# Optimization experiments

Measured on AMD Instinct MI355X. Metric: run time of the kernel, lower is better.

Reference implementation:

```python
import jax, jax.numpy as jnp
import numpy as np

B, LC, LQ, D = 64, 512, 64, 256

def setup_inputs() -> dict:
    key = jax.random.key(0)
    k1, k2, k3, k4 = jax.random.split(key, 4)
    contex = jax.random.normal(k1, (B, LC, D), dtype=jnp.float32)
    question = jax.random.normal(k2, (B, LQ, D), dtype=jnp.float32)
    W_weight = jax.random.normal(k3, (1, 3 * D), dtype=jnp.float32) * (1.0 / np.sqrt(3 * D))
    W_bias = jax.random.normal(k4, (1,), dtype=jnp.float32) * 0.01
    return {"contex": contex, "question": question, "W_weight": W_weight, "W_bias": W_bias}

def reference(contex, question, W_weight, W_bias):
    d = contex.shape[-1]
    w = W_weight[0]  # [3D]; cat order in original is [q, c, q*c]
    wq, wc, wi = w[:d], w[d:2 * d], w[2 * d:]
    # S[b,i,j] = c_i.wc + q_j.wq + (c_i*q_j).wi + bias  (trilinear decomposition)
    s_c = contex @ wc                                   # [B, Lc]
    s_q = question @ wq                                 # [B, Lq]
    s_i = jnp.einsum('bid,bjd->bij', contex * wi, question)  # [B, Lc, Lq]
    S = s_i + s_c[:, :, None] + s_q[:, None, :] + W_bias[0]
    S1 = jax.nn.softmax(S, axis=2)                      # over question
    S2 = jax.nn.softmax(S, axis=1)                      # over context
    A = jnp.einsum('bij,bjd->bid', S1, question)        # [B, Lc, D]
    S3 = jnp.einsum('bij,bkj->bik', S1, S2)             # [B, Lc, Lc]
    Bm = jnp.einsum('bik,bkd->bid', S3, contex)         # [B, Lc, D]
    out = jnp.concatenate([contex, A, contex * A, contex * Bm], axis=2)  # [B, Lc, 4D]
    return out  # dropout is identity at inference
```

## Files before the change

### kernel.cpp

```cpp
#include <hip/hip_runtime.h>

#define BB 64
#define LCC 512
#define LQQ 64
#define DDD 256

typedef short bf16x8 __attribute__((ext_vector_type(8)));
typedef float f32x4 __attribute__((ext_vector_type(4)));

__device__ __forceinline__ unsigned short f2bf(float f) {
  union { float f; unsigned u; } v; v.f = f;
  unsigned u = v.u;
  return (unsigned short)((u + 0x7fffu + ((u >> 16) & 1u)) >> 16);
}
__device__ __forceinline__ float bf2f(unsigned u16) {
  union { unsigned u; float f; } v; v.u = u16 << 16;
  return v.f;
}

__global__ __launch_bounds__(256) void k1_scores(
    const float* __restrict__ cx, const float* __restrict__ qu,
    const float* __restrict__ W, const float* __restrict__ Wb,
    unsigned short* __restrict__ E, unsigned short* __restrict__ Et,
    float* __restrict__ rinv)
{
  __shared__ float w_lds[768];
  __shared__ unsigned short As[128 * 72];
  __shared__ unsigned short Bs[64 * 72];
  __shared__ float E_lds[128 * 65];
  __shared__ float sc_lds[128];
  __shared__ float sq_lds[64];
  float* red = E_lds;

  const int tid = threadIdx.x;
  const int b  = blockIdx.x >> 2;
  const int i0 = (blockIdx.x & 3) * 128;
  const int w = tid >> 6, lane = tid & 63, quad = lane >> 4, ln = lane & 15;

  for (int idx = tid; idx < 768; idx += 256) w_lds[idx] = W[idx];
  __syncthreads();

  {
    const int i = tid >> 1, h = tid & 1;
    const float4* src = (const float4*)(cx + ((size_t)(b * LCC + i0 + i)) * DDD + h * 128);
    const float* wc = w_lds + 256 + h * 128;
    float s = 0.f;
#pragma unroll
    for (int u = 0; u < 32; ++u) {
      float4 v = src[u];
      s += v.x * wc[u*4+0] + v.y * wc[u*4+1] + v.z * wc[u*4+2] + v.w * wc[u*4+3];
    }
    red[tid] = s;
  }
  __syncthreads();
  if (tid < 128) sc_lds[tid] = red[2*tid] + red[2*tid+1];
  __syncthreads();
  if (tid < 128) {
    const int j = tid >> 1, h = tid & 1;
    const float4* src = (const float4*)(qu + ((size_t)(b * LQQ + j)) * DDD + h * 128);
    const float* wq = w_lds + h * 128;
    float s = 0.f;
#pragma unroll
    for (int u = 0; u < 32; ++u) {
      float4 v = src[u];
      s += v.x * wq[u*4+0] + v.y * wq[u*4+1] + v.z * wq[u*4+2] + v.w * wq[u*4+3];
    }
    red[tid] = s;
  }
  __syncthreads();
  if (tid < 64) sq_lds[tid] = red[2*tid] + red[2*tid+1];

  f32x4 acc[2][4];
#pragma unroll
  for (int a = 0; a < 2; ++a)
#pragma unroll
    for (int c = 0; c < 4; ++c) acc[a][c] = (f32x4){0.f, 0.f, 0.f, 0.f};

  for (int kk = 0; kk < 4; ++kk) {
    __syncthreads();
    {
      const int i = tid >> 1, h = tid & 1;
      const float4* src = (const float4*)(cx + ((size_t)(b * LCC + i0 + i)) * DDD + kk * 64 + h * 32);
      const float* wi = w_lds + 512 + kk * 64 + h * 32;
      unsigned short* dst = As + i * 72 + h * 32;
#pragma unroll
      for (int u = 0; u < 8; ++u) {
        float4 v = src[u];
        ushort4 o;
        o.x = f2bf(v.x * wi[u*4+0]);
        o.y = f2bf(v.y * wi[u*4+1]);
        o.z = f2bf(v.z * wi[u*4+2]);
        o.w = f2bf(v.w * wi[u*4+3]);
        *(ushort4*)(dst + u * 4) = o;
      }
    }
    {
      const int j = tid >> 2, c = tid & 3;
      const float4* src = (const float4*)(qu + ((size_t)(b * LQQ + j)) * DDD + kk * 64 + c * 16);
      unsigned short* dst = Bs + j * 72 + c * 16;
#pragma unroll
      for (int u = 0; u < 4; ++u) {
        float4 v = src[u];
        ushort4 o = { f2bf(v.x), f2bf(v.y), f2bf(v.z), f2bf(v.w) };
        *(ushort4*)(dst + u * 4) = o;
      }
    }
    __syncthreads();
#pragma unroll
    for (int ks = 0; ks < 2; ++ks) {
      bf16x8 af[2];
#pragma unroll
      for (int tm = 0; tm < 2; ++tm)
        af[tm] = *(const bf16x8*)(As + (w * 32 + tm * 16 + ln) * 72 + ks * 32 + quad * 8);
#pragma unroll
      for (int tn = 0; tn < 4; ++tn) {
        bf16x8 bf = *(const bf16x8*)(Bs + (tn * 16 + ln) * 72 + ks * 32 + quad * 8);
#pragma unroll
        for (int tm = 0; tm < 2; ++tm)
          acc[tm][tn] = __builtin_amdgcn_mfma_f32_16x16x32_bf16(af[tm], bf, acc[tm][tn], 0, 0, 0);
      }
    }
  }

  const float bias = Wb[0];
  __syncthreads();
#pragma unroll
  for (int tm = 0; tm < 2; ++tm)
#pragma unroll
    for (int tn = 0; tn < 4; ++tn)
#pragma unroll
      for (int r = 0; r < 4; ++r) {
        int il = w * 32 + tm * 16 + quad * 4 + r;
        int j  = tn * 16 + ln;
        float e = __expf(acc[tm][tn][r] + sc_lds[il] + sq_lds[j] + bias);
        E_lds[il * 65 + j] = e;
      }
  __syncthreads();
  if (tid < 128) {
    float s = 0.f;
#pragma unroll
    for (int j = 0; j < 64; ++j) s += E_lds[tid * 65 + j];
    rinv[b * LCC + i0 + tid] = 1.0f / s;
  }
  {
    const int i = tid >> 1, h = tid & 1;
    unsigned short* dst = E + ((size_t)(b * LCC + i0 + i)) * 64 + h * 32;
    const float* srcr = E_lds + i * 65 + h * 32;
#pragma unroll
    for (int u = 0; u < 8; ++u) {
      ushort4 o = { f2bf(srcr[u*4+0]), f2bf(srcr[u*4+1]), f2bf(srcr[u*4+2]), f2bf(srcr[u*4+3]) };
      *(ushort4*)(dst + u * 4) = o;
    }
  }
  {
    const int j = tid >> 2, c = tid & 3;
    unsigned short* dst = Et + ((size_t)(b * LQQ + j)) * LCC + i0 + c * 32;
#pragma unroll
    for (int u = 0; u < 8; ++u) {
      ushort4 o;
      o.x = f2bf(E_lds[(c*32 + u*4 + 0) * 65 + j]);
      o.y = f2bf(E_lds[(c*32 + u*4 + 1) * 65 + j]);
      o.z = f2bf(E_lds[(c*32 + u*4 + 2) * 65 + j]);
      o.w = f2bf(E_lds[(c*32 + u*4 + 3) * 65 + j]);
      *(ushort4*)(dst + u * 4) = o;
    }
  }
}

__global__ __launch_bounds__(256) void k2_tmat(
    const float* __restrict__ cx, const float* __restrict__ qu,
    const unsigned short* __restrict__ Et,
    unsigned short* __restrict__ Qt, unsigned short* __restrict__ Tt)
{
  __shared__ unsigned short As2[64 * 72];
  __shared__ unsigned short Bs2[64 * 72];
  __shared__ float Tl[64 * 65];
  __shared__ float cs_lds[64];

  const int tid = threadIdx.x;
  const int b  = blockIdx.x >> 2;
  const int d0 = (blockIdx.x & 3) * 64;
  const int w = tid >> 6, lane = tid & 63, quad = lane >> 4, ln = lane & 15;

  {
    const int j = tid >> 2, c = tid & 3;
    const float4* src = (const float4*)(qu + ((size_t)(b * LQQ + j)) * DDD + d0 + c * 16);
#pragma unroll
    for (int u = 0; u < 4; ++u) {
      float4 v = src[u];
      Tl[j * 65 + c*16 + u*4 + 0] = v.x;
      Tl[j * 65 + c*16 + u*4 + 1] = v.y;
      Tl[j * 65 + c*16 + u*4 + 2] = v.z;
      Tl[j * 65 + c*16 + u*4 + 3] = v.w;
    }
  }
  __syncthreads();
  {
    const int d = tid & 63, cj = tid >> 6;
    unsigned short* dst = Qt + ((size_t)(b * DDD + d0 + d)) * 64 + cj * 16;
#pragma unroll
    for (int u = 0; u < 4; ++u) {
      ushort4 o;
      o.x = f2bf(Tl[(cj*16 + u*4 + 0) * 65 + d]);
      o.y = f2bf(Tl[(cj*16 + u*4 + 1) * 65 + d]);
      o.z = f2bf(Tl[(cj*16 + u*4 + 2) * 65 + d]);
      o.w = f2bf(Tl[(cj*16 + u*4 + 3) * 65 + d]);
      *(ushort4*)(dst + u * 4) = o;
    }
  }

  f32x4 acc[4];
#pragma unroll
  for (int c = 0; c < 4; ++c) acc[c] = (f32x4){0.f, 0.f, 0.f, 0.f};
  float csp = 0.f;

  const int sj = tid >> 2, sc = tid & 3;
  const int si = tid & 63, sc2 = tid >> 6;

  for (int kk = 0; kk < 8; ++kk) {
    __syncthreads();
    {
      const uint4* src = (const uint4*)(Et + ((size_t)(b * LQQ + sj)) * LCC + kk * 64 + sc * 16);
#pragma unroll
      for (int u = 0; u < 2; ++u) {
        uint4 raw = src[u];
        *(uint4*)(As2 + sj * 72 + sc * 16 + u * 8) = raw;
        csp += bf2f(raw.x & 0xffffu) + bf2f(raw.x >> 16)
             + bf2f(raw.y & 0xffffu) + bf2f(raw.y >> 16)
             + bf2f(raw.z & 0xffffu) + bf2f(raw.z >> 16)
             + bf2f(raw.w & 0xffffu) + bf2f(raw.w >> 16);
      }
    }
    {
      const float4* src = (const float4*)(cx + ((size_t)(b * LCC + kk * 64 + si)) * DDD + d0 + sc2 * 16);
#pragma unroll
      for (int u = 0; u < 4; ++u) {
        float4 v = src[u];
        Bs2[(sc2*16 + u*4 + 0) * 72 + si] = f2bf(v.x);
        Bs2[(sc2*16 + u*4 + 1) * 72 + si] = f2bf(v.y);
        Bs2[(sc2*16 + u*4 + 2) * 72 + si] = f2bf(v.z);
        Bs2[(sc2*16 + u*4 + 3) * 72 + si] = f2bf(v.w);
      }
    }
    __syncthreads();
#pragma unroll
    for (int ks = 0; ks < 2; ++ks) {
      bf16x8 af = *(const bf16x8*)(As2 + (w * 16 + ln) * 72 + ks * 32 + quad * 8);
#pragma unroll
      for (int tn = 0; tn < 4; ++tn) {
        bf16x8 bf = *(const bf16x8*)(Bs2 + (tn * 16 + ln) * 72 + ks * 32 + quad * 8);
        acc[tn] = __builtin_amdgcn_mfma_f32_16x16x32_bf16(af, bf, acc[tn], 0, 0, 0);
      }
    }
  }

  __syncthreads();
  Tl[tid] = csp;
  __syncthreads();
  if (tid < 64) {
    float s = Tl[4*tid] + Tl[4*tid+1] + Tl[4*tid+2] + Tl[4*tid+3];
    cs_lds[tid] = 1.0f / s;
  }
  __syncthreads();
#pragma unroll
  for (int tn = 0; tn < 4; ++tn)
#pragma unroll
    for (int r = 0; r < 4; ++r) {
      int jl = w * 16 + quad * 4 + r;
      Tl[jl * 65 + tn * 16 + ln] = acc[tn][r] * cs_lds[jl];
    }
  __syncthreads();
  {
    const int d = tid & 63, cj = tid >> 6;
    unsigned short* dst = Tt + ((size_t)(b * DDD + d0 + d)) * 64 + cj * 16;
#pragma unroll
    for (int u = 0; u < 4; ++u) {
      ushort4 o;
      o.x = f2bf(Tl[(cj*16 + u*4 + 0) * 65 + d]);
      o.y = f2bf(Tl[(cj*16 + u*4 + 1) * 65 + d]);
      o.z = f2bf(Tl[(cj*16 + u*4 + 2) * 65 + d]);
      o.w = f2bf(Tl[(cj*16 + u*4 + 3) * 65 + d]);
      *(ushort4*)(dst + u * 4) = o;
    }
  }
}

__global__ __launch_bounds__(256) void k3_out(
    const float* __restrict__ cx,
    const unsigned short* __restrict__ E,
    const unsigned short* __restrict__ Qt,
    const unsigned short* __restrict__ Tt,
    const float* __restrict__ rinv,
    float* __restrict__ out)
{
  __shared__ unsigned short As3[64 * 72];
  __shared__ unsigned short Bs3[256 * 72];
  __shared__ float ri_lds[64];

  const int tid = threadIdx.x;
  const int bid = blockIdx.x;
  const int b    = bid >> 4;
  const int it   = (bid >> 1) & 7;
  const int half = bid & 1;
  const int i0 = it * 64;
  const int w = tid >> 6, lane = tid & 63, quad = lane >> 4, ln = lane & 15;

  {
    const int i = tid >> 2, c = tid & 3;
    const uint4* src = (const uint4*)(E + ((size_t)(b * LCC + i0 + i)) * 64 + c * 16);
#pragma unroll
    for (int u = 0; u < 2; ++u)
      *(uint4*)(As3 + i * 72 + c * 16 + u * 8) = src[u];
  }
  {
    const unsigned short* Bsrc = half ? Tt : Qt;
    const int nb = tid & 63, c2 = tid >> 6;
#pragma unroll
    for (int rr = 0; rr < 4; ++rr) {
      int n = rr * 64 + nb;
      const uint4* src = (const uint4*)(Bsrc + ((size_t)(b * DDD + n)) * 64 + c2 * 16);
#pragma unroll
      for (int u = 0; u < 2; ++u)
        *(uint4*)(Bs3 + n * 72 + c2 * 16 + u * 8) = src[u];
    }
  }
  if (tid < 64) ri_lds[tid] = rinv[b * LCC + i0 + tid];
  __syncthreads();

  f32x4 acc[4][4];
#pragma unroll
  for (int a = 0; a < 4; ++a)
#pragma unroll
    for (int c = 0; c < 4; ++c) acc[a][c] = (f32x4){0.f, 0.f, 0.f, 0.f};

#pragma unroll
  for (int ks = 0; ks < 2; ++ks) {
    bf16x8 af[4], bf[4];
#pragma unroll
    for (int tm = 0; tm < 4; ++tm)
      af[tm] = *(const bf16x8*)(As3 + (tm * 16 + ln) * 72 + ks * 32 + quad * 8);
#pragma unroll
    for (int tn = 0; tn < 4; ++tn)
      bf[tn] = *(const bf16x8*)(Bs3 + (w * 64 + tn * 16 + ln) * 72 + ks * 32 + quad * 8);
#pragma unroll
    for (int tm = 0; tm < 4; ++tm)
#pragma unroll
      for (int tn = 0; tn < 4; ++tn)
        acc[tm][tn] = __builtin_amdgcn_mfma_f32_16x16x32_bf16(af[tm], bf[tn], acc[tm][tn], 0, 0, 0);
  }

  const float* cxb = cx + (size_t)b * LCC * DDD;
  float* ob = out + (size_t)b * LCC * 1024;
#pragma unroll
  for (int tm = 0; tm < 4; ++tm)
#pragma unroll
    for (int tn = 0; tn < 4; ++tn)
#pragma unroll
      for (int r = 0; r < 4; ++r) {
        int il = tm * 16 + quad * 4 + r;
        int i = i0 + il;
        int n = w * 64 + tn * 16 + ln;
        float v = acc[tm][tn][r] * ri_lds[il];
        float c = cxb[(size_t)i * DDD + n];
        if (half == 0) {
          ob[(size_t)i * 1024 + 256 + n] = v;
          ob[(size_t)i * 1024 + 512 + n] = c * v;
        } else {
          ob[(size_t)i * 1024 + n]       = c;
          ob[(size_t)i * 1024 + 768 + n] = c * v;
        }
      }
}

extern "C" void kernel_launch(void* const* d_in, const int* in_sizes, int n_in,
                              void* d_out, int out_size, void* d_ws, size_t ws_size,
                              hipStream_t stream) {
  const float* cx = (const float*)d_in[0];
  const float* qu = (const float*)d_in[1];
  const float* W  = (const float*)d_in[2];
  const float* Wb = (const float*)d_in[3];
  float* out = (float*)d_out;

  char* wsb = (char*)d_ws;
  unsigned short* E   = (unsigned short*)(wsb);
  unsigned short* Et  = (unsigned short*)(wsb + (4ull << 20));
  unsigned short* Qt  = (unsigned short*)(wsb + (8ull << 20));
  unsigned short* Tt  = (unsigned short*)(wsb + (10ull << 20));
  float*          ri  = (float*)(wsb + (12ull << 20));

  k1_scores<<<dim3(256), dim3(256), 0, stream>>>(cx, qu, W, Wb, E, Et, ri);
  k2_tmat  <<<dim3(256), dim3(256), 0, stream>>>(cx, qu, Et, Qt, Tt);
  k3_out   <<<dim3(1024), dim3(256), 0, stream>>>(cx, E, Qt, Tt, ri, out);
}
```

Before: 208.6 us.

## Fuse score projections into GEMM staging and vectorize output stores via LDS

In the scores kernel, the c·wc and q·wq row projections are now accumulated while the context and question tiles are staged for the MFMA. This drops the separate pre-pass that read each row a second time, and the row-sum reduction now uses all 256 threads. In the output kernel, accumulator fragments are transposed through LDS (reusing the B-operand buffer) so each thread writes contiguous float4 rows for the output and reads context as float4. The cost is extra LDS traffic and barriers per 16-row chunk.

New measurement: 199.6 us. 1.04x faster.

```diff
diff --git a/kernel.cpp b/kernel.cpp
--- a/kernel.cpp
+++ b/kernel.cpp
@@ -30,7 +30,6 @@
   __shared__ float E_lds[128 * 65];
   __shared__ float sc_lds[128];
   __shared__ float sq_lds[64];
-  float* red = E_lds;
 
   const int tid = threadIdx.x;
   const int b  = blockIdx.x >> 2;
@@ -38,37 +37,6 @@
   const int w = tid >> 6, lane = tid & 63, quad = lane >> 4, ln = lane & 15;
 
   for (int idx = tid; idx < 768; idx += 256) w_lds[idx] = W[idx];
-  __syncthreads();
-
-  {
-    const int i = tid >> 1, h = tid & 1;
-    const float4* src = (const float4*)(cx + ((size_t)(b * LCC + i0 + i)) * DDD + h * 128);
-    const float* wc = w_lds + 256 + h * 128;
-    float s = 0.f;
-#pragma unroll
-    for (int u = 0; u < 32; ++u) {
-      float4 v = src[u];
-      s += v.x * wc[u*4+0] + v.y * wc[u*4+1] + v.z * wc[u*4+2] + v.w * wc[u*4+3];
-    }
-    red[tid] = s;
-  }
-  __syncthreads();
-  if (tid < 128) sc_lds[tid] = red[2*tid] + red[2*tid+1];
-  __syncthreads();
-  if (tid < 128) {
-    const int j = tid >> 1, h = tid & 1;
-    const float4* src = (const float4*)(qu + ((size_t)(b * LQQ + j)) * DDD + h * 128);
-    const float* wq = w_lds + h * 128;
-    float s = 0.f;
-#pragma unroll
-    for (int u = 0; u < 32; ++u) {
-      float4 v = src[u];
-      s += v.x * wq[u*4+0] + v.y * wq[u*4+1] + v.z * wq[u*4+2] + v.w * wq[u*4+3];
-    }
-    red[tid] = s;
-  }
-  __syncthreads();
-  if (tid < 64) sq_lds[tid] = red[2*tid] + red[2*tid+1];
 
   f32x4 acc[2][4];
 #pragma unroll
@@ -76,16 +44,22 @@
 #pragma unroll
     for (int c = 0; c < 4; ++c) acc[a][c] = (f32x4){0.f, 0.f, 0.f, 0.f};
 
+  float scp = 0.f;
+  float sqp = 0.f;
+  const int ai = tid >> 1, ah = tid & 1;
+  const int bj = tid >> 2, bc = tid & 3;
+
   for (int kk = 0; kk < 4; ++kk) {
     __syncthreads();
     {
-      const int i = tid >> 1, h = tid & 1;
-      const float4* src = (const float4*)(cx + ((size_t)(b * LCC + i0 + i)) * DDD + kk * 64 + h * 32);
-      const float* wi = w_lds + 512 + kk * 64 + h * 32;
-      unsigned short* dst = As + i * 72 + h * 32;
+      const float4* src = (const float4*)(cx + ((size_t)(b * LCC + i0 + ai)) * DDD + kk * 64 + ah * 32);
+      const float* wi = w_lds + 512 + kk * 64 + ah * 32;
+      const float* wc = w_lds + 256 + kk * 64 + ah * 32;
+      unsigned short* dst = As + ai * 72 + ah * 32;
 #pragma unroll
       for (int u = 0; u < 8; ++u) {
         float4 v = src[u];
+        scp += v.x * wc[u*4+0] + v.y * wc[u*4+1] + v.z * wc[u*4+2] + v.w * wc[u*4+3];
         ushort4 o;
         o.x = f2bf(v.x * wi[u*4+0]);
         o.y = f2bf(v.y * wi[u*4+1]);
@@ -95,12 +69,13 @@
       }
     }
     {
-      const int j = tid >> 2, c = tid & 3;
-      const float4* src = (const float4*)(qu + ((size_t)(b * LQQ + j)) * DDD + kk * 64 + c * 16);
-      unsigned short* dst = Bs + j * 72 + c * 16;
+      const float4* src = (const float4*)(qu + ((size_t)(b * LQQ + bj)) * DDD + kk * 64 + bc * 16);
+      const float* wq = w_lds + kk * 64 + bc * 16;
+      unsigned short* dst = Bs + bj * 72 + bc * 16;
 #pragma unroll
       for (int u = 0; u < 4; ++u) {
         float4 v = src[u];
+        sqp += v.x * wq[u*4+0] + v.y * wq[u*4+1] + v.z * wq[u*4+2] + v.w * wq[u*4+3];
         ushort4 o = { f2bf(v.x), f2bf(v.y), f2bf(v.z), f2bf(v.w) };
         *(ushort4*)(dst + u * 4) = o;
       }
@@ -122,8 +97,17 @@
     }
   }
 
+  __syncthreads();
+  w_lds[tid] = scp;
+  w_lds[256 + tid] = sqp;
+  __syncthreads();
+  if (tid < 128) sc_lds[tid] = w_lds[2*tid] + w_lds[2*tid+1];
+  if (tid < 64)
+    sq_lds[tid] = w_lds[256 + 4*tid] + w_lds[256 + 4*tid+1]
+                + w_lds[256 + 4*tid+2] + w_lds[256 + 4*tid+3];
   const float bias = Wb[0];
   __syncthreads();
+
 #pragma unroll
   for (int tm = 0; tm < 2; ++tm)
 #pragma unroll
@@ -136,16 +120,18 @@
         E_lds[il * 65 + j] = e;
       }
   __syncthreads();
-  if (tid < 128) {
+  {
     float s = 0.f;
 #pragma unroll
-    for (int j = 0; j < 64; ++j) s += E_lds[tid * 65 + j];
-    rinv[b * LCC + i0 + tid] = 1.0f / s;
-  }
-  {
-    const int i = tid >> 1, h = tid & 1;
-    unsigned short* dst = E + ((size_t)(b * LCC + i0 + i)) * 64 + h * 32;
-    const float* srcr = E_lds + i * 65 + h * 32;
+    for (int j = 0; j < 32; ++j) s += E_lds[ai * 65 + ah * 32 + j];
+    w_lds[tid] = s;
+  }
+  __syncthreads();
+  if (tid < 128) rinv[b * LCC + i0 + tid] = 1.0f / (w_lds[2*tid] + w_lds[2*tid+1]);
+
+  {
+    unsigned short* dst = E + ((size_t)(b * LCC + i0 + ai)) * 64 + ah * 32;
+    const float* srcr = E_lds + ai * 65 + ah * 32;
 #pragma unroll
     for (int u = 0; u < 8; ++u) {
       ushort4 o = { f2bf(srcr[u*4+0]), f2bf(srcr[u*4+1]), f2bf(srcr[u*4+2]), f2bf(srcr[u*4+3]) };
@@ -153,15 +139,14 @@
     }
   }
   {
-    const int j = tid >> 2, c = tid & 3;
-    unsigned short* dst = Et + ((size_t)(b * LQQ + j)) * LCC + i0 + c * 32;
+    unsigned short* dst = Et + ((size_t)(b * LQQ + bj)) * LCC + i0 + bc * 32;
 #pragma unroll
     for (int u = 0; u < 8; ++u) {
       ushort4 o;
-      o.x = f2bf(E_lds[(c*32 + u*4 + 0) * 65 + j]);
-      o.y = f2bf(E_lds[(c*32 + u*4 + 1) * 65 + j]);
-      o.z = f2bf(E_lds[(c*32 + u*4 + 2) * 65 + j]);
-      o.w = f2bf(E_lds[(c*32 + u*4 + 3) * 65 + j]);
+      o.x = f2bf(E_lds[(bc*32 + u*4 + 0) * 65 + bj]);
+      o.y = f2bf(E_lds[(bc*32 + u*4 + 1) * 65 + bj]);
+      o.z = f2bf(E_lds[(bc*32 + u*4 + 2) * 65 + bj]);
+      o.w = f2bf(E_lds[(bc*32 + u*4 + 3) * 65 + bj]);
       *(ushort4*)(dst + u * 4) = o;
     }
   }
@@ -294,8 +279,10 @@
     float* __restrict__ out)
 {
   __shared__ unsigned short As3[64 * 72];
-  __shared__ unsigned short Bs3[256 * 72];
+  __shared__ char BsTr[256 * 72 * 2];
   __shared__ float ri_lds[64];
+  unsigned short* Bs3 = (unsigned short*)BsTr;
+  float* Tr = (float*)BsTr;
 
   const int tid = threadIdx.x;
   const int bid = blockIdx.x;
@@ -351,25 +338,36 @@
 
   const float* cxb = cx + (size_t)b * LCC * DDD;
   float* ob = out + (size_t)b * LCC * 1024;
-#pragma unroll
-  for (int tm = 0; tm < 4; ++tm)
+  const int row = tid >> 4;
+  const int fq  = tid & 15;
+
+#pragma unroll
+  for (int tm = 0; tm < 4; ++tm) {
+    __syncthreads();
 #pragma unroll
     for (int tn = 0; tn < 4; ++tn)
 #pragma unroll
       for (int r = 0; r < 4; ++r) {
-        int il = tm * 16 + quad * 4 + r;
-        int i = i0 + il;
-        int n = w * 64 + tn * 16 + ln;
-        float v = acc[tm][tn][r] * ri_lds[il];
-        float c = cxb[(size_t)i * DDD + n];
-        if (half == 0) {
-          ob[(size_t)i * 1024 + 256 + n] = v;
-          ob[(size_t)i * 1024 + 512 + n] = c * v;
-        } else {
-          ob[(size_t)i * 1024 + n]       = c;
-          ob[(size_t)i * 1024 + 768 + n] = c * v;
-        }
-      }
+        int rloc = quad * 4 + r;
+        Tr[rloc * 260 + w * 64 + tn * 16 + ln] = acc[tm][tn][r] * ri_lds[tm * 16 + rloc];
+      }
+    __syncthreads();
+    const int i = i0 + tm * 16 + row;
+#pragma unroll
+    for (int u = 0; u < 4; ++u) {
+      int c0 = (fq + u * 16) * 4;
+      float4 v = *(const float4*)(Tr + row * 260 + c0);
+      float4 c = *(const float4*)(cxb + (size_t)i * DDD + c0);
+      float4 cv = { c.x * v.x, c.y * v.y, c.z * v.z, c.w * v.w };
+      if (half == 0) {
+        *(float4*)(ob + (size_t)i * 1024 + 256 + c0) = v;
+        *(float4*)(ob + (size_t)i * 1024 + 512 + c0) = cv;
+      } else {
+        *(float4*)(ob + (size_t)i * 1024 + c0)       = c;
+        *(float4*)(ob + (size_t)i * 1024 + 768 + c0) = cv;
+      }
+    }
+  }
 }
 
 extern "C" void kernel_launch(void* const* d_in, const int* in_sizes, int n_in,
```
